# Performance work log

Hardware: AMD Instinct MI355X
Metric: run time of the kernel (lower is better)

The kernel has to match this reference:

```python
import jax, jax.numpy as jnp
import numpy as np
from jax import lax

B, M = 16384, 128
NUM_LAYERS, OW, OH = 22, 11, 11
MAX_VEC = np.array([9.0, 1.0, 1.0, 10.0, 3.0, 254.0, 1.0, 1.0, 235.0, 8.0, 9.0, 250.0,
                    29.0, 1.0, 1.0, 8.0, 1.0, 1.0, 6.0, 3.0, 1.0, 2.0], dtype=np.float32)


def setup_inputs() -> dict:
    key = jax.random.key(0)
    ks = jax.random.split(key, 20)
    s = 0.05
    return {
        "observations": jax.random.randint(ks[0], (B, M, 3), 0, 255, dtype=jnp.int32),
        "cnn1_w": jax.random.normal(ks[1], (64, 22, 5, 5), jnp.float32) * s,
        "cnn1_b": jnp.zeros((64,), jnp.float32),
        "cnn2_w": jax.random.normal(ks[2], (64, 64, 3, 3), jnp.float32) * s,
        "cnn2_b": jnp.zeros((64,), jnp.float32),
        "fc1_w": jax.random.normal(ks[3], (128, 64), jnp.float32) * s,
        "fc1_b": jnp.zeros((128,), jnp.float32),
        "enc_w": jax.random.normal(ks[4], (128, 128), jnp.float32) * s,
        "enc_b": jnp.zeros((128,), jnp.float32),
        "critic1_w": jax.random.normal(ks[5], (1024, 128), jnp.float32) * s,
        "critic1_b": jnp.zeros((1024,), jnp.float32),
        "value_w": jax.random.normal(ks[6], (1, 1024), jnp.float32) * s,
        "value_b": jnp.zeros((1,), jnp.float32),
        "actor1_w": jax.random.normal(ks[7], (512, 128), jnp.float32) * s,
        "actor1_b": jnp.zeros((512,), jnp.float32),
        "action_emb": jax.random.normal(ks[8], (100, 16), jnp.float32) * s,
        "head0_w": jax.random.normal(ks[9], (9, 528), jnp.float32) * s,
        "head0_b": jnp.zeros((9,), jnp.float32),
        "head1_w": jax.random.normal(ks[10], (10, 528), jnp.float32) * s,
        "head1_b": jnp.zeros((10,), jnp.float32),
    }


def _encode_scatter(observations):
    # zero-out any byte equal to 255 (matches torch in-place masking)
    tok = jnp.where(observations == 255, 0, observations)  # [B, M, 3]
    coords = tok[..., 0].astype(jnp.uint8)
    x = ((coords >> 4) & 15).astype(jnp.int32)
    y = (coords & 15).astype(jnp.int32)
    atr = tok[..., 1].astype(jnp.int32)
    val = tok[..., 2].astype(jnp.float32)
    b, m = atr.shape
    valid = (x < OW) & (y < OH) & (atr < NUM_LAYERS)
    b_idx = jnp.broadcast_to(jnp.arange(b, dtype=jnp.int32)[:, None], (b, m))
    b_idx = jnp.where(valid, b_idx, b)  # route invalid tokens out of bounds -> dropped
    box = jnp.zeros((b, NUM_LAYERS, OW, OH), jnp.float32)
    box = box.at[b_idx, atr, x, y].set(val, mode="drop")
    return box


def _forward(observations, cnn1_w, cnn1_b, cnn2_w, cnn2_b, fc1_w, fc1_b, enc_w, enc_b,
             critic1_w, critic1_b, value_w, value_b, actor1_w, actor1_b, action_emb,
             head0_w, head0_b, head1_w, head1_b):
    box = _encode_scatter(observations)
    x = box / jnp.asarray(MAX_VEC)[None, :, None, None]
    dn = ("NCHW", "OIHW", "NCHW")
    x = lax.conv_general_dilated(x, cnn1_w, (3, 3), "VALID", dimension_numbers=dn) + cnn1_b[None, :, None, None]
    x = lax.conv_general_dilated(x, cnn2_w, (1, 1), "VALID", dimension_numbers=dn) + cnn2_b[None, :, None, None]
    x = x.reshape(x.shape[0], -1)                 # [B, 64]
    x = x @ fc1_w.T + fc1_b                       # [B, 128]
    hidden = x @ enc_w.T + enc_b                  # [B, 128]
    critic = jnp.tanh(hidden @ critic1_w.T + critic1_b)
    value = critic @ value_w.T + value_b          # [B, 1]
    actor = hidden @ actor1_w.T + actor1_b        # [B, 512]
    emb = jnp.broadcast_to(action_emb.mean(axis=0)[None, :], (actor.shape[0], action_emb.shape[1]))
    comb = jnp.concatenate([actor, emb], axis=-1)  # [B, 528]
    logits = jnp.concatenate([comb @ head0_w.T + head0_b, comb @ head1_w.T + head1_b], axis=-1)
    return logits, value


def reference(observations, cnn1_w, cnn1_b, cnn2_w, cnn2_b, fc1_w, fc1_b, enc_w, enc_b,
              critic1_w, critic1_b, value_w, value_b, actor1_w, actor1_b, action_emb,
              head0_w, head0_b, head1_w, head1_b):
    return _forward(observations, cnn1_w, cnn1_b, cnn2_w, cnn2_b, fc1_w, fc1_b, enc_w, enc_b,
                    critic1_w, critic1_b, value_w, value_b, actor1_w, actor1_b, action_emb,
                    head0_w, head0_b, head1_w, head1_b)
```

## Files before the change

### kernel.cpp

```cpp
#include <hip/hip_runtime.h>
#include <math.h>

#define NB 16384
#define NTOK 128
#define NKEY 2662
#define NLOG 19
#define TB 16

typedef __attribute__((ext_vector_type(8))) short short8;
typedef __attribute__((ext_vector_type(4))) float floatx4;

__device__ __constant__ float c_maxv[22] = {
    9.f, 1.f, 1.f, 10.f, 3.f, 254.f, 1.f, 1.f, 235.f, 8.f, 9.f, 250.f,
    29.f, 1.f, 1.f, 8.f, 1.f, 1.f, 6.f, 3.f, 1.f, 2.f};

__device__ __forceinline__ unsigned short f2bf(float f) {
    unsigned u = __float_as_uint(f);
    return (unsigned short)((u + 0x7FFFu + ((u >> 16) & 1u)) >> 16);
}
__device__ __forceinline__ float tanh_fast(float x) {
    float e = __builtin_amdgcn_exp2f(x * 2.885390082f);
    return 1.f - 2.f * __builtin_amdgcn_rcpf(e + 1.f);
}

__global__ __launch_bounds__(256) void k_pre1(
    const float* __restrict__ w1, const float* __restrict__ b1,
    const float* __restrict__ w2, const float* __restrict__ b2,
    const float* __restrict__ fc1w, const float* __restrict__ encw,
    const float* __restrict__ h0w, const float* __restrict__ h1w,
    const float* __restrict__ a1w, const float* __restrict__ aemb,
    const float* __restrict__ c1w,
    float* __restrict__ G, float* __restrict__ E,
    float* __restrict__ h2b, float* __restrict__ emb,
    float* __restrict__ Wlog, unsigned short* __restrict__ c1wb)
{
    __shared__ float s_w2[72 * 65];
    const int bid = blockIdx.x, t = threadIdx.x;
    if (bid < 666) {
        const int v = t & 63;
        const int key_u = __builtin_amdgcn_readfirstlane(bid * 4 + (t >> 6));
        const int key_c = (key_u < NKEY) ? key_u : (NKEY - 1);
        const int c = key_c / 121, rem = key_c % 121, X = rem / 11, Y = rem % 11;
        float acc = 0.f;
        for (int u0 = 0; u0 < 64; u0 += 8) {
            __syncthreads();
            #pragma unroll
            for (int r = 0; r < 18; ++r) {
                int g = t + 256 * r;
                int vg = g / 72, rg = g % 72;
                s_w2[rg * 65 + vg] = w2[vg * 576 + u0 * 9 + rg];
            }
            __syncthreads();
            #pragma unroll
            for (int ur = 0; ur < 8; ++ur) {
                const int w1base = (u0 + ur) * 550 + c * 25;
                #pragma unroll
                for (int i = 0; i < 3; ++i) {
                    int xi = X - 3 * i;
                    if (xi < 0 || xi > 4) continue;
                    #pragma unroll
                    for (int j = 0; j < 3; ++j) {
                        int yj = Y - 3 * j;
                        if (yj < 0 || yj > 4) continue;
                        acc += s_w2[(ur * 9 + i * 3 + j) * 65 + v] *
                               w1[w1base + xi * 5 + yj];
                    }
                }
            }
        }
        if (key_u < NKEY) G[key_u * 64 + v] = acc;
    } else if (bid < 698) {
        int m = (bid - 666) * 256 + t;
        int h = __builtin_amdgcn_readfirstlane(m >> 6) & 127;
        int v = t & 63;
        float acc = 0.f;
        #pragma unroll 8
        for (int p = 0; p < 128; ++p)
            acc += encw[h * 128 + p] * fc1w[p * 64 + v];
        E[v * 128 + h] = acc;
    } else if (bid == 698) {
        if (t < 64) {
            float s = b2[t];
            for (int u = 0; u < 64; ++u) {
                float ws = 0.f;
                for (int k = 0; k < 9; ++k) ws += w2[(t * 64 + u) * 9 + k];
                s += b1[u] * ws;
            }
            h2b[t] = s;
        } else if (t < 80) {
            int e = t - 64;
            float s = 0.f;
            for (int r = 0; r < 100; ++r) s += aemb[r * 16 + e];
            emb[e] = s * 0.01f;
        }
    } else if (bid < 709) {
        int n = (bid - 699) * 256 + t;
        if (n < NLOG * 128) {
            int o = __builtin_amdgcn_readfirstlane(n >> 7);
            int h = n & 127;
            const float* hw = (o < 9) ? (h0w + o * 528) : (h1w + (o - 9) * 528);
            float acc = 0.f;
            #pragma unroll 8
            for (int a = 0; a < 512; ++a)
                acc += hw[a] * a1w[a * 128 + h];
            Wlog[n] = acc;
        }
    } else {
        int n = (bid - 709) * 256 + t;
        c1wb[n] = f2bf(c1w[n]);
    }
}

__global__ __launch_bounds__(256) void k_pre2(
    const float* __restrict__ G, const float* __restrict__ E,
    const float* __restrict__ h2b, const float* __restrict__ emb,
    const float* __restrict__ fc1w, const float* __restrict__ fc1b,
    const float* __restrict__ encw, const float* __restrict__ encb,
    const float* __restrict__ a1b,
    const float* __restrict__ h0w, const float* __restrict__ h0b,
    const float* __restrict__ h1w, const float* __restrict__ h1b,
    float* __restrict__ Weff, float* __restrict__ beff, float* __restrict__ blog)
{
    const int bid = blockIdx.x, t = threadIdx.x;
    if (bid < 1331) {
        int n = bid * 256 + t;
        int key = __builtin_amdgcn_readfirstlane(n >> 7);
        int h = n & 127;
        float acc = 0.f;
        #pragma unroll 8
        for (int v = 0; v < 64; ++v)
            acc += E[v * 128 + h] * G[key * 64 + v];
        Weff[n] = acc / c_maxv[key / 121];
    } else {
        __shared__ float s_t[128];
        if (t < 128) {
            float s = fc1b[t];
            for (int v = 0; v < 64; ++v) s += fc1w[t * 64 + v] * h2b[v];
            s_t[t] = s;
        }
        __syncthreads();
        if (t < 128) {
            float s = encb[t];
            for (int p = 0; p < 128; ++p) s += encw[t * 128 + p] * s_t[p];
            beff[t] = s;
        } else if (t < 128 + NLOG) {
            int o = t - 128;
            float s = (o < 9) ? h0b[o] : h1b[o - 9];
            for (int a = 0; a < 512; ++a) {
                float hw = (o < 9) ? h0w[o * 528 + a] : h1w[(o - 9) * 528 + a];
                s += hw * a1b[a];
            }
            for (int e = 0; e < 16; ++e) {
                float hw = (o < 9) ? h0w[o * 528 + 512 + e] : h1w[(o - 9) * 528 + 512 + e];
                s += hw * emb[e];
            }
            blog[o] = s;
        }
    }
}

__global__ __launch_bounds__(256) void k_main(
    const int* __restrict__ obs,
    const float* __restrict__ Weff, const float* __restrict__ beff,
    const unsigned short* __restrict__ c1wb, const float* __restrict__ c1b,
    const float* __restrict__ vw, const float* __restrict__ vb,
    const float* __restrict__ Wlog, const float* __restrict__ blog,
    float* __restrict__ out)
{
    __shared__ int            s_lst[TB * 32];
    __shared__ float          s_hidden[TB * 128];
    __shared__ unsigned short s_hb[TB * 136];
    __shared__ int            s_cnt[TB];
    __shared__ float          s_val[64];

    const int tid = threadIdx.x, bid = blockIdx.x;
    const int b0 = bid * TB;

    if (tid < TB) s_cnt[tid] = 0;
    __syncthreads();

    {
        const int gtok0 = b0 * NTOK;
        #pragma unroll
        for (int k = 0; k < TB * NTOK / 256; ++k) {
            int tt = tid + 256 * k;
            int gi = (gtok0 + tt) * 3;
            int o0 = obs[gi], o1 = obs[gi + 1], o2 = obs[gi + 2];
            o0 = (o0 == 255) ? 0 : o0;
            o1 = (o1 == 255) ? 0 : o1;
            o2 = (o2 == 255) ? 0 : o2;
            int x = (o0 >> 4) & 15, y = o0 & 15;
            if (x < 11 && y < 11 && o1 < 22) {
                int bb = tt >> 7, m = tt & 127;
                int pos = atomicAdd(&s_cnt[bb], 1);
                if (pos < 32)
                    s_lst[bb * 32 + pos] = (m << 20) | (o2 << 12) | (o1 * 121 + x * 11 + y);
            }
        }
    }
    __syncthreads();

    {
        int bb = tid >> 4, e0 = tid & 15;
        int n = s_cnt[bb]; if (n > 32) n = 32;
        #pragma unroll
        for (int r = 0; r < 2; ++r) {
            int e = e0 + 16 * r;
            if (e < n) {
                int p = s_lst[bb * 32 + e];
                bool dead = false;
                for (int i = 0; i < n; ++i) {
                    int q = s_lst[bb * 32 + i];
                    dead |= (((q ^ p) & 0xFFF) == 0) && (q > p);
                }
                if (dead) s_lst[bb * 32 + e] = p & ~0x000FF000;
            }
        }
    }
    __syncthreads();

    {
        int h = tid & 127, bg = tid >> 7;
        for (int bb = bg; bb < TB; bb += 2) {
            float acc = beff[h];
            int n = s_cnt[bb]; if (n > 32) n = 32;
            for (int i = 0; i < n; ++i) {
                int p = s_lst[bb * 32 + i];
                acc += (float)((p >> 12) & 0xFF) * Weff[(p & 0xFFF) * 128 + h];
            }
            s_hidden[bb * 128 + h] = acc;
            s_hb[bb * 136 + h] = f2bf(acc);
        }
    }
    __syncthreads();

    {
        const int lane = tid & 63, w = tid >> 6;
        const int lm = lane & 15, quad = lane >> 4;
        short8 af[4];
        #pragma unroll
        for (int kk = 0; kk < 4; ++kk)
            af[kk] = *(const short8*)&s_hb[lm * 136 + kk * 32 + quad * 8];

        float vpart[4] = {0.f, 0.f, 0.f, 0.f};
        for (int nt = 0; nt < 16; ++nt) {
            int j = w * 256 + nt * 16 + lm;
            floatx4 acc = {0.f, 0.f, 0.f, 0.f};
            #pragma unroll
            for (int kk = 0; kk < 4; ++kk) {
                short8 bf = *(const short8*)&c1wb[j * 128 + kk * 32 + quad * 8];
                acc = __builtin_amdgcn_mfma_f32_16x16x32_bf16(af[kk], bf, acc, 0, 0, 0);
            }
            float bj = c1b[j], wj = vw[j];
            #pragma unroll
            for (int r = 0; r < 4; ++r)
                vpart[r] += tanh_fast(acc[r] + bj) * wj;
        }
        #pragma unroll
        for (int off = 1; off <= 8; off <<= 1)
            #pragma unroll
            for (int r = 0; r < 4; ++r)
                vpart[r] += __shfl_xor(vpart[r], off, 64);
        if (lm == 0) {
            #pragma unroll
            for (int r = 0; r < 4; ++r)
                s_val[w * 16 + quad * 4 + r] = vpart[r];
        }
    }
    __syncthreads();
    if (tid < TB) {
        float v = s_val[tid] + s_val[16 + tid] + s_val[32 + tid] + s_val[48 + tid];
        out[NB * NLOG + b0 + tid] = v + vb[0];
    }

    {
        const float4* s_h4 = (const float4*)s_hidden;
        const float4* wl4  = (const float4*)Wlog;
        int bl = tid >> 4, oo = tid & 15;
        #pragma unroll
        for (int rep = 0; rep < 2; ++rep) {
            int o = oo + rep * 16;
            if (o < NLOG) {
                float acc = blog[o];
                #pragma unroll
                for (int hq = 0; hq < 32; ++hq) {
                    float4 hv = s_h4[bl * 32 + hq];
                    float4 wl = wl4[o * 32 + hq];
                    acc += wl.x * hv.x + wl.y * hv.y + wl.z * hv.z + wl.w * hv.w;
                }
                out[(b0 + bl) * NLOG + o] = acc;
            }
        }
    }
}

extern "C" void kernel_launch(void* const* d_in, const int* in_sizes, int n_in,
                              void* d_out, int out_size, void* d_ws, size_t ws_size,
                              hipStream_t stream)
{
    const int*   obs  = (const int*)  d_in[0];
    const float* w1   = (const float*)d_in[1];
    const float* b1   = (const float*)d_in[2];
    const float* w2   = (const float*)d_in[3];
    const float* b2   = (const float*)d_in[4];
    const float* fc1w = (const float*)d_in[5];
    const float* fc1b = (const float*)d_in[6];
    const float* encw = (const float*)d_in[7];
    const float* encb = (const float*)d_in[8];
    const float* c1w  = (const float*)d_in[9];
    const float* c1b  = (const float*)d_in[10];
    const float* vw   = (const float*)d_in[11];
    const float* vb   = (const float*)d_in[12];
    const float* a1w  = (const float*)d_in[13];
    const float* a1b  = (const float*)d_in[14];
    const float* aemb = (const float*)d_in[15];
    const float* h0w  = (const float*)d_in[16];
    const float* h0b  = (const float*)d_in[17];
    const float* h1w  = (const float*)d_in[18];
    const float* h1b  = (const float*)d_in[19];

    float* W    = (float*)d_ws;
    float* G    = W;
    float* E    = W + 170368;
    float* h2b  = W + 178560;
    float* emb  = W + 178624;
    float* Weff = W + 178640;
    float* beff = W + 519376;
    float* Wlog = W + 519504;
    float* blog = W + 521936;
    unsigned short* c1wb = (unsigned short*)(W + 524288);

    hipLaunchKernelGGL(k_pre1, dim3(1221), dim3(256), 0, stream,
                       w1, b1, w2, b2, fc1w, encw, h0w, h1w, a1w, aemb, c1w,
                       G, E, h2b, emb, Wlog, c1wb);
    hipLaunchKernelGGL(k_pre2, dim3(1332), dim3(256), 0, stream,
                       G, E, h2b, emb, fc1w, fc1b, encw, encb, a1b,
                       h0w, h0b, h1w, h1b, Weff, beff, blog);
    hipLaunchKernelGGL(k_main, dim3(NB / TB), dim3(256), 0, stream,
                       obs, Weff, beff, c1wb, c1b, vw, vb, Wlog, blog,
                       (float*)d_out);
}
```

Measured before the change: 211.6 us.

## Refactor weight-folding preprocessing and halve main-kernel batch tile

Reorders the weight-folding chain so fc1 is first folded into the conv2 weights (W2Ft), then combined with conv1 weights and the transposed encoder matrix in a second kernel, replacing the previous G/E decomposition. The bias and logit-bias work is merged into the first pre-kernel, and the c1w bf16 conversion is packed into fewer blocks. The main kernel drops to 8 samples per block with an occupancy hint and loads each token as a 12-byte struct. The MFMA tile is kept at 16 rows, with the unused half zero-padded, at the cost of wasted MFMA work.

```diff
diff --git a/kernel.cpp b/kernel.cpp
--- a/kernel.cpp
+++ b/kernel.cpp
@@ -5,10 +5,12 @@
 #define NTOK 128
 #define NKEY 2662
 #define NLOG 19
-#define TB 16
+#define TB 8
 
 typedef __attribute__((ext_vector_type(8))) short short8;
 typedef __attribute__((ext_vector_type(4))) float floatx4;
+
+struct Tok3 { int x, y, z; };
 
 __device__ __constant__ float c_maxv[22] = {
     9.f, 1.f, 1.f, 10.f, 3.f, 254.f, 1.f, 1.f, 235.f, 8.f, 9.f, 250.f,
@@ -23,62 +25,46 @@
     return 1.f - 2.f * __builtin_amdgcn_rcpf(e + 1.f);
 }
 
-__global__ __launch_bounds__(256) void k_pre1(
+__global__ __launch_bounds__(256) void k_preA(
     const float* __restrict__ w1, const float* __restrict__ b1,
     const float* __restrict__ w2, const float* __restrict__ b2,
-    const float* __restrict__ fc1w, const float* __restrict__ encw,
-    const float* __restrict__ h0w, const float* __restrict__ h1w,
-    const float* __restrict__ a1w, const float* __restrict__ aemb,
+    const float* __restrict__ fc1w, const float* __restrict__ fc1b,
+    const float* __restrict__ encw, const float* __restrict__ encb,
+    const float* __restrict__ a1w, const float* __restrict__ a1b,
+    const float* __restrict__ aemb,
+    const float* __restrict__ h0w, const float* __restrict__ h0b,
+    const float* __restrict__ h1w, const float* __restrict__ h1b,
     const float* __restrict__ c1w,
-    float* __restrict__ G, float* __restrict__ E,
-    float* __restrict__ h2b, float* __restrict__ emb,
+    float* __restrict__ W2Ft, float* __restrict__ encwT,
+    float* __restrict__ beff, float* __restrict__ blog,
     float* __restrict__ Wlog, unsigned short* __restrict__ c1wb)
 {
-    __shared__ float s_w2[72 * 65];
+    __shared__ float sF[64 * 129];
     const int bid = blockIdx.x, t = threadIdx.x;
-    if (bid < 666) {
-        const int v = t & 63;
-        const int key_u = __builtin_amdgcn_readfirstlane(bid * 4 + (t >> 6));
-        const int key_c = (key_u < NKEY) ? key_u : (NKEY - 1);
-        const int c = key_c / 121, rem = key_c % 121, X = rem / 11, Y = rem % 11;
-        float acc = 0.f;
-        for (int u0 = 0; u0 < 64; u0 += 8) {
-            __syncthreads();
-            #pragma unroll
-            for (int r = 0; r < 18; ++r) {
-                int g = t + 256 * r;
-                int vg = g / 72, rg = g % 72;
-                s_w2[rg * 65 + vg] = w2[vg * 576 + u0 * 9 + rg];
-            }
-            __syncthreads();
-            #pragma unroll
-            for (int ur = 0; ur < 8; ++ur) {
-                const int w1base = (u0 + ur) * 550 + c * 25;
-                #pragma unroll
-                for (int i = 0; i < 3; ++i) {
-                    int xi = X - 3 * i;
-                    if (xi < 0 || xi > 4) continue;
-                    #pragma unroll
-                    for (int j = 0; j < 3; ++j) {
-                        int yj = Y - 3 * j;
-                        if (yj < 0 || yj > 4) continue;
-                        acc += s_w2[(ur * 9 + i * 3 + j) * 65 + v] *
-                               w1[w1base + xi * 5 + yj];
-                    }
-                }
-            }
-        }
-        if (key_u < NKEY) G[key_u * 64 + v] = acc;
-    } else if (bid < 698) {
-        int m = (bid - 666) * 256 + t;
-        int h = __builtin_amdgcn_readfirstlane(m >> 6) & 127;
-        int v = t & 63;
-        float acc = 0.f;
-        #pragma unroll 8
-        for (int p = 0; p < 128; ++p)
-            acc += encw[h * 128 + p] * fc1w[p * 64 + v];
-        E[v * 128 + h] = acc;
-    } else if (bid == 698) {
+
+    if (bid < 72) {
+        #pragma unroll
+        for (int r = 0; r < 32; ++r) {
+            int idx = t + 256 * r;
+            int p_ = idx >> 6, v_ = idx & 63;
+            sF[v_ * 129 + p_] = fc1w[idx];
+        }
+        __syncthreads();
+        #pragma unroll
+        for (int r = 0; r < 4; ++r) {
+            int idx = t + 256 * r;
+            int p = idx & 127;
+            int uk = __builtin_amdgcn_readfirstlane(bid * 8 + (idx >> 7));
+            float acc = 0.f;
+            #pragma unroll 8
+            for (int v = 0; v < 64; ++v)
+                acc += sF[v * 129 + p] * w2[v * 576 + uk];
+            W2Ft[uk * 128 + p] = acc;
+        }
+    } else if (bid == 72) {
+        float* s_h2b = sF;
+        float* s_emb = sF + 64;
+        float* s_t   = sF + 80;
         if (t < 64) {
             float s = b2[t];
             for (int u = 0; u < 64; ++u) {
@@ -86,56 +72,17 @@
                 for (int k = 0; k < 9; ++k) ws += w2[(t * 64 + u) * 9 + k];
                 s += b1[u] * ws;
             }
-            h2b[t] = s;
+            s_h2b[t] = s;
         } else if (t < 80) {
             int e = t - 64;
             float s = 0.f;
             for (int r = 0; r < 100; ++r) s += aemb[r * 16 + e];
-            emb[e] = s * 0.01f;
-        }
-    } else if (bid < 709) {
-        int n = (bid - 699) * 256 + t;
-        if (n < NLOG * 128) {
-            int o = __builtin_amdgcn_readfirstlane(n >> 7);
-            int h = n & 127;
-            const float* hw = (o < 9) ? (h0w + o * 528) : (h1w + (o - 9) * 528);
-            float acc = 0.f;
-            #pragma unroll 8
-            for (int a = 0; a < 512; ++a)
-                acc += hw[a] * a1w[a * 128 + h];
-            Wlog[n] = acc;
-        }
-    } else {
-        int n = (bid - 709) * 256 + t;
-        c1wb[n] = f2bf(c1w[n]);
-    }
-}
-
-__global__ __launch_bounds__(256) void k_pre2(
-    const float* __restrict__ G, const float* __restrict__ E,
-    const float* __restrict__ h2b, const float* __restrict__ emb,
-    const float* __restrict__ fc1w, const float* __restrict__ fc1b,
-    const float* __restrict__ encw, const float* __restrict__ encb,
-    const float* __restrict__ a1b,
-    const float* __restrict__ h0w, const float* __restrict__ h0b,
-    const float* __restrict__ h1w, const float* __restrict__ h1b,
-    float* __restrict__ Weff, float* __restrict__ beff, float* __restrict__ blog)
-{
-    const int bid = blockIdx.x, t = threadIdx.x;
-    if (bid < 1331) {
-        int n = bid * 256 + t;
-        int key = __builtin_amdgcn_readfirstlane(n >> 7);
-        int h = n & 127;
-        float acc = 0.f;
-        #pragma unroll 8
-        for (int v = 0; v < 64; ++v)
-            acc += E[v * 128 + h] * G[key * 64 + v];
-        Weff[n] = acc / c_maxv[key / 121];
-    } else {
-        __shared__ float s_t[128];
+            s_emb[e] = s * 0.01f;
+        }
+        __syncthreads();
         if (t < 128) {
             float s = fc1b[t];
-            for (int v = 0; v < 64; ++v) s += fc1w[t * 64 + v] * h2b[v];
+            for (int v = 0; v < 64; ++v) s += fc1w[t * 64 + v] * s_h2b[v];
             s_t[t] = s;
         }
         __syncthreads();
@@ -152,14 +99,74 @@
             }
             for (int e = 0; e < 16; ++e) {
                 float hw = (o < 9) ? h0w[o * 528 + 512 + e] : h1w[(o - 9) * 528 + 512 + e];
-                s += hw * emb[e];
+                s += hw * s_emb[e];
             }
             blog[o] = s;
         }
-    }
-}
-
-__global__ __launch_bounds__(256) void k_main(
+    } else if (bid < 83) {
+        int n = (bid - 73) * 256 + t;
+        if (n < NLOG * 128) {
+            int o = __builtin_amdgcn_readfirstlane(n >> 7);
+            int h = n & 127;
+            const float* hw = (o < 9) ? (h0w + o * 528) : (h1w + (o - 9) * 528);
+            float acc = 0.f;
+            #pragma unroll 8
+            for (int a = 0; a < 512; ++a)
+                acc += hw[a] * a1w[a * 128 + h];
+            Wlog[n] = acc;
+        }
+    } else if (bid < 99) {
+        #pragma unroll
+        for (int r = 0; r < 32; ++r) {
+            int n = (bid - 83) * 8192 + t + 256 * r;
+            c1wb[n] = f2bf(c1w[n]);
+        }
+    } else {
+        #pragma unroll
+        for (int r = 0; r < 8; ++r) {
+            int idx = (bid - 99) * 2048 + t + 256 * r;
+            int h = idx >> 7, p = idx & 127;
+            encwT[p * 128 + h] = encw[idx];
+        }
+    }
+}
+
+__global__ __launch_bounds__(256) void k_preB(
+    const float* __restrict__ W2Ft, const float* __restrict__ w1,
+    const float* __restrict__ encwT, float* __restrict__ Weff)
+{
+    __shared__ float sA[2][128];
+    const int t = threadIdx.x, bid = blockIdx.x;
+    const int half = t >> 7, p = t & 127;
+    const int key = __builtin_amdgcn_readfirstlane(bid * 2 + half);
+    const int c = key / 121, rem = key % 121, X = rem / 11, Y = rem % 11;
+
+    float acc = 0.f;
+    for (int u = 0; u < 64; ++u) {
+        const float* w1u = w1 + u * 550 + c * 25;
+        #pragma unroll
+        for (int i = 0; i < 3; ++i) {
+            int xi = X - 3 * i;
+            if (xi < 0 || xi > 4) continue;
+            #pragma unroll
+            for (int j = 0; j < 3; ++j) {
+                int yj = Y - 3 * j;
+                if (yj < 0 || yj > 4) continue;
+                acc += w1u[xi * 5 + yj] * W2Ft[(u * 9 + i * 3 + j) * 128 + p];
+            }
+        }
+    }
+    sA[half][p] = acc / c_maxv[c];
+    __syncthreads();
+
+    float o = 0.f;
+    #pragma unroll 8
+    for (int p2 = 0; p2 < 128; ++p2)
+        o += encwT[p2 * 128 + p] * sA[half][p2];
+    Weff[key * 128 + p] = o;
+}
+
+__global__ __launch_bounds__(256, 8) void k_main(
     const int* __restrict__ obs,
     const float* __restrict__ Weff, const float* __restrict__ beff,
     const unsigned short* __restrict__ c1wb, const float* __restrict__ c1b,
@@ -169,7 +176,7 @@
 {
     __shared__ int            s_lst[TB * 32];
     __shared__ float          s_hidden[TB * 128];
-    __shared__ unsigned short s_hb[TB * 136];
+    __shared__ unsigned short s_hb[16 * 136];
     __shared__ int            s_cnt[TB];
     __shared__ float          s_val[64];
 
@@ -177,18 +184,19 @@
     const int b0 = bid * TB;
 
     if (tid < TB) s_cnt[tid] = 0;
-    __syncthreads();
-
-    {
+    for (int i = tid; i < 8 * 136; i += 256) s_hb[8 * 136 + i] = 0;
+    __syncthreads();
+
+    {
+        const Tok3* obs3 = (const Tok3*)obs;
         const int gtok0 = b0 * NTOK;
         #pragma unroll
         for (int k = 0; k < TB * NTOK / 256; ++k) {
             int tt = tid + 256 * k;
-            int gi = (gtok0 + tt) * 3;
-            int o0 = obs[gi], o1 = obs[gi + 1], o2 = obs[gi + 2];
-            o0 = (o0 == 255) ? 0 : o0;
-            o1 = (o1 == 255) ? 0 : o1;
-            o2 = (o2 == 255) ? 0 : o2;
+            Tok3 o = obs3[gtok0 + tt];
+            int o0 = (o.x == 255) ? 0 : o.x;
+            int o1 = (o.y == 255) ? 0 : o.y;
+            int o2 = (o.z == 255) ? 0 : o.z;
             int x = (o0 >> 4) & 15, y = o0 & 15;
             if (x < 11 && y < 11 && o1 < 22) {
                 int bb = tt >> 7, m = tt & 127;
@@ -201,20 +209,16 @@
     __syncthreads();
 
     {
-        int bb = tid >> 4, e0 = tid & 15;
+        int bb = tid >> 5, e = tid & 31;
         int n = s_cnt[bb]; if (n > 32) n = 32;
-        #pragma unroll
-        for (int r = 0; r < 2; ++r) {
-            int e = e0 + 16 * r;
-            if (e < n) {
-                int p = s_lst[bb * 32 + e];
-                bool dead = false;
-                for (int i = 0; i < n; ++i) {
-                    int q = s_lst[bb * 32 + i];
-                    dead |= (((q ^ p) & 0xFFF) == 0) && (q > p);
-                }
-                if (dead) s_lst[bb * 32 + e] = p & ~0x000FF000;
-            }
+        if (e < n) {
+            int p = s_lst[bb * 32 + e];
+            bool dead = false;
+            for (int i = 0; i < n; ++i) {
+                int q = s_lst[bb * 32 + i];
+                dead |= (((q ^ p) & 0xFFF) == 0) && (q > p);
+            }
+            if (dead) s_lst[bb * 32 + e] = p & ~0x000FF000;
         }
     }
     __syncthreads();
@@ -276,20 +280,16 @@
     {
         const float4* s_h4 = (const float4*)s_hidden;
         const float4* wl4  = (const float4*)Wlog;
-        int bl = tid >> 4, oo = tid & 15;
-        #pragma unroll
-        for (int rep = 0; rep < 2; ++rep) {
-            int o = oo + rep * 16;
-            if (o < NLOG) {
-                float acc = blog[o];
-                #pragma unroll
-                for (int hq = 0; hq < 32; ++hq) {
-                    float4 hv = s_h4[bl * 32 + hq];
-                    float4 wl = wl4[o * 32 + hq];
-                    acc += wl.x * hv.x + wl.y * hv.y + wl.z * hv.z + wl.w * hv.w;
-                }
-                out[(b0 + bl) * NLOG + o] = acc;
-            }
+        int bl = tid >> 5, o = tid & 31;
+        if (o < NLOG) {
+            float acc = blog[o];
+            #pragma unroll
+            for (int hq = 0; hq < 32; ++hq) {
+                float4 hv = s_h4[bl * 32 + hq];
+                float4 wl = wl4[o * 32 + hq];
+                acc += wl.x * hv.x + wl.y * hv.y + wl.z * hv.z + wl.w * hv.w;
+            }
+            out[(b0 + bl) * NLOG + o] = acc;
         }
     }
 }
@@ -319,23 +319,21 @@
     const float* h1w  = (const float*)d_in[18];
     const float* h1b  = (const float*)d_in[19];
 
-    float* W    = (float*)d_ws;
-    float* G    = W;
-    float* E    = W + 170368;
-    float* h2b  = W + 178560;
-    float* emb  = W + 178624;
-    float* Weff = W + 178640;
-    float* beff = W + 519376;
-    float* Wlog = W + 519504;
-    float* blog = W + 521936;
-    unsigned short* c1wb = (unsigned short*)(W + 524288);
-
-    hipLaunchKernelGGL(k_pre1, dim3(1221), dim3(256), 0, stream,
-                       w1, b1, w2, b2, fc1w, encw, h0w, h1w, a1w, aemb, c1w,
-                       G, E, h2b, emb, Wlog, c1wb);
-    hipLaunchKernelGGL(k_pre2, dim3(1332), dim3(256), 0, stream,
-                       G, E, h2b, emb, fc1w, fc1b, encw, encb, a1b,
-                       h0w, h0b, h1w, h1b, Weff, beff, blog);
+    float* W     = (float*)d_ws;
+    float* W2Ft  = W;
+    float* encwT = W + 73728;
+    float* beff  = W + 90112;
+    float* blog  = W + 90240;
+    float* Wlog  = W + 90272;
+    float* Weff  = W + 92704;
+    unsigned short* c1wb = (unsigned short*)(W + 433440);
+
+    hipLaunchKernelGGL(k_preA, dim3(107), dim3(256), 0, stream,
+                       w1, b1, w2, b2, fc1w, fc1b, encw, encb, a1w, a1b, aemb,
+                       h0w, h0b, h1w, h1b, c1w,
+                       W2Ft, encwT, beff, blog, Wlog, c1wb);
+    hipLaunchKernelGGL(k_preB, dim3(1331), dim3(256), 0, stream,
+                       W2Ft, w1, encwT, Weff);
     hipLaunchKernelGGL(k_main, dim3(NB / TB), dim3(256), 0, stream,
                        obs, Weff, beff, c1wb, c1b, vw, vb, Wlog, blog,
                        (float*)d_out);
```

Result: slower. 264.3 us (+24.9%).
